# Kernel optimization log

Measured on AMD Instinct MI355X. Metric: run time of the kernel, lower is better.

Reference implementation:

```python
import jax, jax.numpy as jnp
import numpy as np

B, G, C = 512, 8192, 6
REGION_NUM = 1024


def setup_inputs() -> dict:
    key = jax.random.key(0)
    k1, k2, k3 = jax.random.split(key, 3)
    # points clustered at ~5cm scale so some fall inside the gripper box
    group_points = jax.random.normal(k1, (B, G, C), jnp.float32) * 0.05
    group_index = jax.random.randint(k2, (B, G), 0, 100000, dtype=jnp.int32)
    grasp = jax.random.normal(k3, (B, 7), jnp.float32) * 0.05
    return {
        "group_points": group_points,
        "group_index": group_index,
        "grasp": grasp,
        "widths": jnp.float32(0.08),
        "height": jnp.float32(0.04),
        "depths": jnp.float32(0.06),
        "region_num": REGION_NUM,
    }


def _normalize_fix(v, fallback):
    # normalize rows of [B,3]; rows with zero norm are replaced by `fallback`
    eps = 1e-12
    n = jnp.linalg.norm(v, axis=1)
    v = v / (n + eps)[:, None]
    return jnp.where((n == 0.0)[:, None], jnp.asarray(fallback, v.dtype), v)


def _transform(group_points, grasp):
    # Per-grasp frame construction + rotation of group points into gripper frame.
    center = grasp[:, 0:3]            # [B,3]
    axis_y = grasp[:, 3:6]            # [B,3]
    angle = grasp[:, 6]               # [B]
    c, s = jnp.cos(angle), jnp.sin(angle)
    zero, one = jnp.zeros_like(c), jnp.ones_like(c)
    # rotation about y by angle: [[c,0,-s],[0,1,0],[s,0,c]]
    R1 = jnp.stack([c, zero, -s, zero, one, zero, s, zero, c], axis=1).reshape(-1, 3, 3)
    axis_y = _normalize_fix(axis_y, [0.0, 1.0, 0.0])
    axis_x = jnp.stack([axis_y[:, 1], -axis_y[:, 0], zero], axis=1)
    axis_x = _normalize_fix(axis_x, [1.0, 0.0, 0.0])
    axis_z = jnp.cross(axis_x, axis_y)
    nz = jnp.linalg.norm(axis_z, axis=1)
    axis_z = axis_z / jnp.where(nz == 0.0, 1.0, nz)[:, None]
    axis_z = jnp.where((nz == 0.0)[:, None], jnp.asarray([0.0, 0.0, 1.0], axis_z.dtype), axis_z)
    M = jnp.stack([axis_x, axis_y, axis_z], axis=2) @ R1   # columns are axes, [B,3,3]
    approach = _normalize_fix(M[:, :, 0], [1.0, 0.0, 0.0])
    minor = jnp.cross(approach, axis_y)
    Mrows = jnp.stack([approach, axis_y, minor], axis=1)    # rows = frame axes, [B,3,3]
    # pcs_t[b,n,:] = Mrows[b] @ (p[b,n] - center[b])
    pcs_t = jnp.einsum('bij,bnj->bni', Mrows, group_points[:, :, :3] - center[:, None, :])
    return pcs_t


def reference(group_points, group_index, grasp, widths, height, depths, region_num):
    pcs_t = _transform(group_points, grasp)              # [B,G,3]
    x_lim, y_lim, z_lim = depths / 2, widths / 2, height / 2
    x, y, z = pcs_t[..., 0], pcs_t[..., 1], pcs_t[..., 2]
    mask = (x > 0) & (x < x_lim) & (y > -y_lim) & (y < y_lim) & (z > -z_lim) & (z < z_lim)  # [B,G]
    count = mask.sum(axis=1)                             # [B]
    # stable sort: indices of in-box points first, in original order
    order = jnp.argsort(jnp.where(mask, 0, 1).astype(jnp.int32), axis=1, stable=True)
    j = jnp.arange(region_num)
    # deterministic compaction: take first region_num hits; wrap (sample with
    # replacement) when fewer than region_num hits are available
    pos = j[None, :] % jnp.maximum(count, 1)[:, None]
    idx = jnp.take_along_axis(order, pos, axis=1)        # [B,region_num]
    valid = count > 5                                    # [B]
    pc = jnp.concatenate(
        [jnp.take_along_axis(pcs_t, idx[:, :, None], axis=1),
         jnp.take_along_axis(group_points[:, :, 3:], idx[:, :, None], axis=1)], axis=-1)
    gripper_pc = jnp.where(valid[:, None, None], pc, -1.0)             # [B,region_num,6]
    gripper_pc_index = jnp.where(valid[:, None], idx, -1)              # [B,region_num]
    gripper_pc_index_inall = jnp.where(
        valid[:, None], jnp.take_along_axis(group_index, idx, axis=1), -1)
    true_mask = valid.astype(jnp.float32)                              # [B]
    return gripper_pc, gripper_pc_index, gripper_pc_index_inall, true_mask
```

## Files before the change

kernel.cpp:

```cpp
#include <hip/hip_runtime.h>


__device__ __forceinline__ float fm(float a, float b) { return __fmul_rn(a, b); }
__device__ __forceinline__ float fa(float a, float b) { return __fadd_rn(a, b); }
__device__ __forceinline__ float fs(float a, float b) { return __fsub_rn(a, b); }
__device__ __forceinline__ float fd(float a, float b) { return __fdiv_rn(a, b); }

extern "C" __global__ void xform_kernel(const float* __restrict__ grasp,
                                        float* __restrict__ xf, int B) {
    int b = blockIdx.x * blockDim.x + threadIdx.x;
    if (b >= B) return;
    const float* gr = grasp + (size_t)b * 7;

    float cx = gr[0], cy = gr[1], cz = gr[2];
    float vx = gr[3], vy = gr[4], vz = gr[5];
    float angle = gr[6];
    float c = (float)cos((double)angle);
    float s = (float)sin((double)angle);

    float n  = __fsqrt_rn(fa(fa(fm(vx, vx), fm(vy, vy)), fm(vz, vz)));
    float dn = fa(n, 1e-12f);
    float ayx = fd(vx, dn), ayy = fd(vy, dn), ayz = fd(vz, dn);
    if (n == 0.0f) { ayx = 0.0f; ayy = 1.0f; ayz = 0.0f; }

    float bx = ayy, by = -ayx;
    float n2  = __fsqrt_rn(fa(fa(fm(bx, bx), fm(by, by)), 0.0f));
    float dn2 = fa(n2, 1e-12f);
    float axx = fd(bx, dn2), axy = fd(by, dn2), axz = fd(0.0f, dn2);
    if (n2 == 0.0f) { axx = 1.0f; axy = 0.0f; axz = 0.0f; }

    float zx = fs(fm(axy, ayz), fm(axz, ayy));
    float zy = fs(fm(axz, ayx), fm(axx, ayz));
    float zz = fs(fm(axx, ayy), fm(axy, ayx));
    float nz = __fsqrt_rn(fa(fa(fm(zx, zx), fm(zy, zy)), fm(zz, zz)));
    float dz = (nz == 0.0f) ? 1.0f : nz;
    zx = fd(zx, dz); zy = fd(zy, dz); zz = fd(zz, dz);
    if (nz == 0.0f) { zx = 0.0f; zy = 0.0f; zz = 1.0f; }

    float px = fa(fm(axx, c), fm(zx, s));
    float py = fa(fm(axy, c), fm(zy, s));
    float pz = fa(fm(axz, c), fm(zz, s));
    float n3  = __fsqrt_rn(fa(fa(fm(px, px), fm(py, py)), fm(pz, pz)));
    float dn3 = fa(n3, 1e-12f);
    float apx = fd(px, dn3), apy = fd(py, dn3), apz = fd(pz, dn3);
    if (n3 == 0.0f) { apx = 1.0f; apy = 0.0f; apz = 0.0f; }

    float mx = fs(fm(apy, ayz), fm(apz, ayy));
    float my = fs(fm(apz, ayx), fm(apx, ayz));
    float mz = fs(fm(apx, ayy), fm(apy, ayx));

    float* o = xf + (size_t)b * 12;
    o[0] = apx; o[1] = apy; o[2]  = apz;
    o[3] = ayx; o[4] = ayy; o[5]  = ayz;
    o[6] = mx;  o[7] = my;  o[8]  = mz;
    o[9] = cx;  o[10] = cy; o[11] = cz;
}

#define NTHREADS 1024
#define NWAVES (NTHREADS / 64)

extern "C" __global__ void __launch_bounds__(NTHREADS)
gripper_kernel(const float* __restrict__ gp,
               const int*   __restrict__ gidx,
               const float* __restrict__ xf,
               const float* __restrict__ widths_p,
               const float* __restrict__ height_p,
               const float* __restrict__ depths_p,
               float* __restrict__ out,
               int B, int G, int RN) {
    const int b    = blockIdx.x;
    const int tid  = threadIdx.x;
    const int lane = tid & 63;
    const int wave = tid >> 6;

    extern __shared__ int s_idx[];
    __shared__ int s_cnt[2][NWAVES];

    const float4 q0 = *(const float4*)(xf + (size_t)b * 12 + 0);
    const float4 q1 = *(const float4*)(xf + (size_t)b * 12 + 4);
    const float4 q2 = *(const float4*)(xf + (size_t)b * 12 + 8);
    const float r0x = q0.x, r0y = q0.y, r0z = q0.z;
    const float r1x = q0.w, r1y = q1.x, r1z = q1.y;
    const float r2x = q1.z, r2y = q1.w, r2z = q2.x;
    const float cx  = q2.y, cy  = q2.z, cz  = q2.w;

    const float x_lim = fm(*depths_p, 0.5f);
    const float y_lim = fm(*widths_p, 0.5f);
    const float z_lim = fm(*height_p, 0.5f);

    const float* __restrict__ gpb = gp + (size_t)b * G * 6;

    int running = 0;
    const int niter = G / NTHREADS;
    for (int it = 0; it < niter; ++it) {
        const int g = it * NTHREADS + tid;
        const float2 l0 = *(const float2*)(gpb + (size_t)g * 6);
        const float2 l1 = *(const float2*)(gpb + (size_t)g * 6 + 2);
        const float dx = fs(l0.x, cx), dy = fs(l0.y, cy), dz = fs(l1.x, cz);
        const float x = fa(fa(fm(r0x, dx), fm(r0y, dy)), fm(r0z, dz));
        const float y = fa(fa(fm(r1x, dx), fm(r1y, dy)), fm(r1z, dz));
        const float z = fa(fa(fm(r2x, dx), fm(r2y, dy)), fm(r2z, dz));
        const bool m = (x > 0.0f) & (x < x_lim) & (y > -y_lim) & (y < y_lim) &
                       (z > -z_lim) & (z < z_lim);

        const unsigned long long bal = __ballot(m);
        if (lane == 0) s_cnt[it & 1][wave] = __popcll(bal);
        __syncthreads();

        int off = running, tot = 0;
        #pragma unroll
        for (int w = 0; w < NWAVES; ++w) {
            const int cw = s_cnt[it & 1][w];
            if (w < wave) off += cw;
            tot += cw;
        }
        const int pos = off + __popcll(bal & ((1ull << lane) - 1ull));
        if (m && pos < RN) s_idx[pos] = g;
        running += tot;
    }
    __syncthreads();

    const int count = running;

    float* __restrict__ out0 = out;
    float* __restrict__ out1 = out + (size_t)B * RN * 6;
    float* __restrict__ out2 = out1 + (size_t)B * RN;
    float* __restrict__ out3 = out2 + (size_t)B * RN;

    if (count > 5) {
        const int m = count < RN ? count : RN;
        for (int j = tid; j < RN; j += NTHREADS) {
            const int i = s_idx[j % m];
            const float* p = gpb + (size_t)i * 6;
            const float2 l0 = *(const float2*)(p);
            const float2 l1 = *(const float2*)(p + 2);
            const float2 l2 = *(const float2*)(p + 4);
            const float dx = fs(l0.x, cx), dy = fs(l0.y, cy), dz = fs(l1.x, cz);
            const float x = fa(fa(fm(r0x, dx), fm(r0y, dy)), fm(r0z, dz));
            const float y = fa(fa(fm(r1x, dx), fm(r1y, dy)), fm(r1z, dz));
            const float z = fa(fa(fm(r2x, dx), fm(r2y, dy)), fm(r2z, dz));
            float* o = out0 + ((size_t)b * RN + j) * 6;
            *(float2*)(o + 0) = make_float2(x, y);
            *(float2*)(o + 2) = make_float2(z, l1.y);
            *(float2*)(o + 4) = l2;
            out1[(size_t)b * RN + j] = (float)i;
            out2[(size_t)b * RN + j] = (float)gidx[(size_t)b * G + i];
        }
        if (tid == 0) out3[b] = 1.0f;
    } else {
        for (int j = tid; j < RN; j += NTHREADS) {
            float* o = out0 + ((size_t)b * RN + j) * 6;
            const float2 neg = make_float2(-1.0f, -1.0f);
            *(float2*)(o + 0) = neg;
            *(float2*)(o + 2) = neg;
            *(float2*)(o + 4) = neg;
            out1[(size_t)b * RN + j] = -1.0f;
            out2[(size_t)b * RN + j] = -1.0f;
        }
        if (tid == 0) out3[b] = 0.0f;
    }
}

extern "C" void kernel_launch(void* const* d_in, const int* in_sizes, int n_in,
                              void* d_out, int out_size, void* d_ws, size_t ws_size,
                              hipStream_t stream) {
    const float* gp     = (const float*)d_in[0];
    const int*   gidx   = (const int*)d_in[1];
    const float* grasp  = (const float*)d_in[2];
    const float* widths = (const float*)d_in[3];
    const float* height = (const float*)d_in[4];
    const float* depths = (const float*)d_in[5];
    float* out = (float*)d_out;
    float* xf  = (float*)d_ws;

    const int B  = in_sizes[2] / 7;
    const int G  = in_sizes[1] / B;
    const int RN = (out_size / B - 1) / 8;

    xform_kernel<<<(B + 255) / 256, 256, 0, stream>>>(grasp, xf, B);

    const size_t smem = (size_t)RN * sizeof(int);
    gripper_kernel<<<B, NTHREADS, smem, stream>>>(gp, gidx, xf, widths,
                                                  height, depths, out, B, G, RN);
}
```

Before: 180.4 us.

## Split gripper kernel into parallel mask pass and scan-based emit pass

Replaces the single per-batch 1024-thread kernel, which looped over G with a block-wide barrier each iteration, with two kernels. The first computes per-64-point ballot masks and counts across many small blocks. The second runs a wave-level prefix scan over the chunk counts to compact the first RN hit indices into shared memory, and splits output emission across four blocks per batch. The aim is more parallelism and fewer serialized barriers, at the cost of an extra launch, a workspace round trip for masks and counts, and the compaction being redone in each of the four emit blocks.

```diff
diff --git a/kernel.cpp b/kernel.cpp
--- a/kernel.cpp
+++ b/kernel.cpp
@@ -56,25 +56,23 @@
     o[9] = cx;  o[10] = cy; o[11] = cz;
 }
 
-#define NTHREADS 1024
-#define NWAVES (NTHREADS / 64)
-
-extern "C" __global__ void __launch_bounds__(NTHREADS)
-gripper_kernel(const float* __restrict__ gp,
-               const int*   __restrict__ gidx,
-               const float* __restrict__ xf,
-               const float* __restrict__ widths_p,
-               const float* __restrict__ height_p,
-               const float* __restrict__ depths_p,
-               float* __restrict__ out,
-               int B, int G, int RN) {
-    const int b    = blockIdx.x;
+#define MT 256
+#define ESPLIT 4
+
+extern "C" __global__ void __launch_bounds__(MT)
+mask_kernel(const float* __restrict__ gp,
+            const float* __restrict__ xf,
+            const float* __restrict__ widths_p,
+            const float* __restrict__ height_p,
+            const float* __restrict__ depths_p,
+            unsigned long long* __restrict__ masks,
+            int* __restrict__ counts,
+            int G) {
+    const int spb  = G >> 8;
+    const int b    = blockIdx.x / spb;
+    const int seg  = blockIdx.x - b * spb;
     const int tid  = threadIdx.x;
     const int lane = tid & 63;
-    const int wave = tid >> 6;
-
-    extern __shared__ int s_idx[];
-    __shared__ int s_cnt[2][NWAVES];
 
     const float4 q0 = *(const float4*)(xf + (size_t)b * 12 + 0);
     const float4 q1 = *(const float4*)(xf + (size_t)b * 12 + 4);
@@ -88,48 +86,98 @@
     const float y_lim = fm(*widths_p, 0.5f);
     const float z_lim = fm(*height_p, 0.5f);
 
-    const float* __restrict__ gpb = gp + (size_t)b * G * 6;
-
-    int running = 0;
-    const int niter = G / NTHREADS;
-    for (int it = 0; it < niter; ++it) {
-        const int g = it * NTHREADS + tid;
-        const float2 l0 = *(const float2*)(gpb + (size_t)g * 6);
-        const float2 l1 = *(const float2*)(gpb + (size_t)g * 6 + 2);
-        const float dx = fs(l0.x, cx), dy = fs(l0.y, cy), dz = fs(l1.x, cz);
-        const float x = fa(fa(fm(r0x, dx), fm(r0y, dy)), fm(r0z, dz));
-        const float y = fa(fa(fm(r1x, dx), fm(r1y, dy)), fm(r1z, dz));
-        const float z = fa(fa(fm(r2x, dx), fm(r2y, dy)), fm(r2z, dz));
-        const bool m = (x > 0.0f) & (x < x_lim) & (y > -y_lim) & (y < y_lim) &
-                       (z > -z_lim) & (z < z_lim);
-
-        const unsigned long long bal = __ballot(m);
-        if (lane == 0) s_cnt[it & 1][wave] = __popcll(bal);
-        __syncthreads();
-
-        int off = running, tot = 0;
-        #pragma unroll
-        for (int w = 0; w < NWAVES; ++w) {
-            const int cw = s_cnt[it & 1][w];
-            if (w < wave) off += cw;
-            tot += cw;
-        }
-        const int pos = off + __popcll(bal & ((1ull << lane) - 1ull));
-        if (m && pos < RN) s_idx[pos] = g;
-        running += tot;
+    const int g = (seg << 8) + tid;
+    const float* p = gp + ((size_t)b * G + (size_t)g) * 6;
+    const float2 l0 = *(const float2*)(p);
+    const float2 l1 = *(const float2*)(p + 2);
+    const float dx = fs(l0.x, cx), dy = fs(l0.y, cy), dz = fs(l1.x, cz);
+    const float x = fa(fa(fm(r0x, dx), fm(r0y, dy)), fm(r0z, dz));
+    const float y = fa(fa(fm(r1x, dx), fm(r1y, dy)), fm(r1z, dz));
+    const float z = fa(fa(fm(r2x, dx), fm(r2y, dy)), fm(r2z, dz));
+    const bool m = (x > 0.0f) & (x < x_lim) & (y > -y_lim) & (y < y_lim) &
+                   (z > -z_lim) & (z < z_lim);
+
+    const unsigned long long bal = __ballot(m);
+    if (lane == 0) {
+        const size_t o = (size_t)b * (G >> 6) + (g >> 6);
+        masks[o]  = bal;
+        counts[o] = __popcll(bal);
+    }
+}
+
+extern "C" __global__ void __launch_bounds__(MT)
+emit_kernel(const float* __restrict__ gp,
+            const int*   __restrict__ gidx,
+            const unsigned long long* __restrict__ masks,
+            const int*   __restrict__ counts,
+            const float* __restrict__ xf,
+            float* __restrict__ out,
+            int B, int G, int RN) {
+    const int b     = blockIdx.x / ESPLIT;
+    const int split = blockIdx.x - b * ESPLIT;
+    const int tid   = threadIdx.x;
+    const int lane  = tid & 63;
+    const int wv    = tid >> 6;
+    const int NCH   = G >> 6;
+
+    __shared__ unsigned long long s_mask[256];
+    __shared__ int s_pref[256];
+    __shared__ int s_total;
+    extern __shared__ int s_idx[];
+
+    for (int c = tid; c < NCH; c += MT)
+        s_mask[c] = masks[(size_t)b * NCH + c];
+
+    if (wv == 0) {
+        int carry = 0;
+        for (int cb = 0; cb < NCH; cb += 64) {
+            const int c = counts[(size_t)b * NCH + cb + lane];
+            int x = c;
+            #pragma unroll
+            for (int d2 = 1; d2 < 64; d2 <<= 1) {
+                int v = __shfl_up(x, d2, 64);
+                if (lane >= d2) x += v;
+            }
+            s_pref[cb + lane] = carry + (x - c);
+            carry += __shfl(x, 63, 64);
+        }
+        if (lane == 0) s_total = carry;
     }
     __syncthreads();
 
-    const int count = running;
+    for (int c = wv; c < NCH; c += (MT / 64)) {
+        const unsigned long long mk = s_mask[c];
+        const int base = s_pref[c];
+        if (mk != 0ull && base < RN) {
+            const int pos = base + __popcll(mk & ((1ull << lane) - 1ull));
+            if (((mk >> lane) & 1ull) && pos < RN) s_idx[pos] = (c << 6) + lane;
+        }
+    }
+    __syncthreads();
+
+    const int count = s_total;
+
+    const float4 q0 = *(const float4*)(xf + (size_t)b * 12 + 0);
+    const float4 q1 = *(const float4*)(xf + (size_t)b * 12 + 4);
+    const float4 q2 = *(const float4*)(xf + (size_t)b * 12 + 8);
+    const float r0x = q0.x, r0y = q0.y, r0z = q0.z;
+    const float r1x = q0.w, r1y = q1.x, r1z = q1.y;
+    const float r2x = q1.z, r2y = q1.w, r2z = q2.x;
+    const float cx  = q2.y, cy  = q2.z, cz  = q2.w;
 
     float* __restrict__ out0 = out;
     float* __restrict__ out1 = out + (size_t)B * RN * 6;
     float* __restrict__ out2 = out1 + (size_t)B * RN;
     float* __restrict__ out3 = out2 + (size_t)B * RN;
 
+    const float* __restrict__ gpb = gp + (size_t)b * G * 6;
+    const int chunk = (RN + ESPLIT - 1) / ESPLIT;
+    const int j0 = split * chunk;
+    const int j1 = (j0 + chunk < RN) ? (j0 + chunk) : RN;
+
     if (count > 5) {
         const int m = count < RN ? count : RN;
-        for (int j = tid; j < RN; j += NTHREADS) {
+        for (int j = j0 + tid; j < j1; j += MT) {
             const int i = s_idx[j % m];
             const float* p = gpb + (size_t)i * 6;
             const float2 l0 = *(const float2*)(p);
@@ -146,9 +194,9 @@
             out1[(size_t)b * RN + j] = (float)i;
             out2[(size_t)b * RN + j] = (float)gidx[(size_t)b * G + i];
         }
-        if (tid == 0) out3[b] = 1.0f;
+        if (split == 0 && tid == 0) out3[b] = 1.0f;
     } else {
-        for (int j = tid; j < RN; j += NTHREADS) {
+        for (int j = j0 + tid; j < j1; j += MT) {
             float* o = out0 + ((size_t)b * RN + j) * 6;
             const float2 neg = make_float2(-1.0f, -1.0f);
             *(float2*)(o + 0) = neg;
@@ -157,7 +205,7 @@
             out1[(size_t)b * RN + j] = -1.0f;
             out2[(size_t)b * RN + j] = -1.0f;
         }
-        if (tid == 0) out3[b] = 0.0f;
+        if (split == 0 && tid == 0) out3[b] = 0.0f;
     }
 }
 
@@ -171,15 +219,24 @@
     const float* height = (const float*)d_in[4];
     const float* depths = (const float*)d_in[5];
     float* out = (float*)d_out;
-    float* xf  = (float*)d_ws;
 
     const int B  = in_sizes[2] / 7;
     const int G  = in_sizes[1] / B;
     const int RN = (out_size / B - 1) / 8;
+    const int NCH = G >> 6;
+
+    float* xf = (float*)d_ws;
+    size_t off = ((size_t)B * 12 * sizeof(float) + 255) & ~(size_t)255;
+    unsigned long long* masks = (unsigned long long*)((char*)d_ws + off);
+    off += (size_t)B * NCH * sizeof(unsigned long long);
+    int* cnts = (int*)((char*)d_ws + off);
 
     xform_kernel<<<(B + 255) / 256, 256, 0, stream>>>(grasp, xf, B);
 
+    mask_kernel<<<B * (G >> 8), MT, 0, stream>>>(gp, xf, widths, height,
+                                                 depths, masks, cnts, G);
+
     const size_t smem = (size_t)RN * sizeof(int);
-    gripper_kernel<<<B, NTHREADS, smem, stream>>>(gp, gidx, xf, widths,
-                                                  height, depths, out, B, G, RN);
-}
+    emit_kernel<<<B * ESPLIT, MT, smem, stream>>>(gp, gidx, masks, cnts, xf,
+                                                  out, B, G, RN);
+}
```

Result: slower. 186.3 us (+3.3%).
